# Performance work log

Measured on AMD Instinct MI355X. Metric: run time of the kernel, lower is better.

## Reference

```python
import math
import jax, jax.numpy as jnp
import numpy as np

GRID = (256, 256, 256)
K = 9                # kernel_size (already odd)
SIGMA = K / 4.0
PAD = K // 2
CLIP = 0.03


def _gaussian_kernel():
    ax = np.arange(K, dtype=np.float32)
    mean = (K - 1) / 2.0
    g = np.exp(-(((ax - mean) / SIGMA) ** 2) / 2.0) / (SIGMA * math.sqrt(2.0 * math.pi))
    k = g[:, None, None] * g[None, :, None] * g[None, None, :]
    k = k / k.sum()
    return jnp.asarray(k, dtype=jnp.float32).reshape(1, 1, K, K, K)  # OIDHW


def setup_inputs() -> dict:
    key = jax.random.key(0)
    x = jax.random.normal(key, (int(np.prod(GRID)),), dtype=jnp.float32)
    kernel = _gaussian_kernel()
    return {"x": x, "kernel": kernel}


def reference(x, kernel):
    v = x.reshape(1, 1, *GRID)  # [1,1,D,H,W]
    # reflect padding (torch padding_mode='reflect', padding = K//2)
    p = jnp.pad(v, ((0, 0), (0, 0), (PAD, PAD), (PAD, PAD), (PAD, PAD)), mode="reflect")
    # torch Conv3d is cross-correlation; lax conv does not flip kernels either
    out = jax.lax.conv_general_dilated(
        p, kernel,
        window_strides=(1, 1, 1),
        padding="VALID",
        dimension_numbers=("NCDHW", "OIDHW", "NCDHW"),
    )
    # clip: keep smoothed output within +/-CLIP of the original input
    out = jnp.maximum(jnp.minimum(v, out + CLIP), out - CLIP)
    return out.reshape(-1)
```

## Files before the change

kernel.cpp:

```cpp
#include <hip/hip_runtime.h>
#include <hip/hip_fp16.h>
#include <math.h>

#define CLIPV 0.03f

struct W9 { float g[9]; };
struct half4 { __half2 a, b; };

__device__ __forceinline__ int reflect_idx(int i, int n) {
    if (i < 0) i = -i;
    if (i >= n) i = 2 * n - 2 - i;
    return i;
}

__device__ __forceinline__ float4 h4_to_f4(half4 v) {
    const float2 ab = __half22float2(v.a), cd = __half22float2(v.b);
    float4 r; r.x = ab.x; r.y = ab.y; r.z = cd.x; r.w = cd.y; return r;
}
__device__ __forceinline__ half4 f4_to_h4(float4 v) {
    half4 r; r.a = __floats2half2_rn(v.x, v.y); r.b = __floats2half2_rn(v.z, v.w);
    return r;
}

__global__ __launch_bounds__(256) void wh_pass(const float* __restrict__ x,
                                               __half* __restrict__ t2, W9 wt) {
    __shared__ __half tile[64][264];

    const int bid = blockIdx.x;
    const int xcd = bid & 7;
    const int k   = bid >> 3;
    const int z   = xcd * 32 + (k >> 2);
    const int rb  = (k & 3) * 64;
    const int wv  = threadIdx.x >> 6;
    const int h0  = rb + wv * 16;
    const int L   = threadIdx.x & 63;
    const int w4  = L * 4;

    const float* plane = x + (size_t)z * 65536;

    {
        float4 ring[9];
        float4 cur = *(const float4*)(plane + (size_t)reflect_idx(h0 - 4, 256) * 256 + w4);
        float4 nxt = *(const float4*)(plane + (size_t)reflect_idx(h0 - 3, 256) * 256 + w4);

        #pragma unroll
        for (int i = 0; i < 24; ++i) {
            float4 nn;
            if (i < 22)
                nn = *(const float4*)(plane + (size_t)reflect_idx(h0 - 2 + i, 256) * 256 + w4);

            ring[i % 9] = cur;

            if (i >= 8) {
                float a0 = 0.f, a1 = 0.f, a2 = 0.f, a3 = 0.f;
                #pragma unroll
                for (int j = 0; j < 9; ++j) {
                    const float4 v = ring[(i - 8 + j) % 9];
                    a0 = fmaf(wt.g[j], v.x, a0);
                    a1 = fmaf(wt.g[j], v.y, a1);
                    a2 = fmaf(wt.g[j], v.z, a2);
                    a3 = fmaf(wt.g[j], v.w, a3);
                }
                float4 o; o.x = a0; o.y = a1; o.z = a2; o.w = a3;
                *(half4*)&tile[wv * 16 + (i - 8)][w4] = f4_to_h4(o);
            }

            cur = nxt; nxt = nn;
        }
    }
    __syncthreads();

    __half* oplane = t2 + (size_t)z * 65536 + (size_t)rb * 256;
    const bool l0 = (L == 0), l63 = (L == 63);
    const int offA = l0  ? w4 : (w4 - 4);
    const int offC = l63 ? w4 : (w4 + 4);

    #pragma unroll
    for (int s = 0; s < 16; ++s) {
        const int r = wv * 16 + s;
        const float4 A = h4_to_f4(*(const half4*)&tile[r][offA]);
        const float4 B = h4_to_f4(*(const half4*)&tile[r][w4]);
        const float4 C = h4_to_f4(*(const half4*)&tile[r][offC]);

        float sv[12];
        sv[0] = l0 ? C.x : A.x;
        sv[1] = l0 ? B.w : A.y;
        sv[2] = l0 ? B.z : A.z;
        sv[3] = l0 ? B.y : A.w;
        sv[4] = B.x; sv[5] = B.y; sv[6] = B.z; sv[7] = B.w;
        sv[8]  = l63 ? B.z : C.x;
        sv[9]  = l63 ? B.y : C.y;
        sv[10] = l63 ? B.x : C.z;
        sv[11] = l63 ? A.w : C.w;

        float a0 = 0.f, a1 = 0.f, a2 = 0.f, a3 = 0.f;
        #pragma unroll
        for (int j = 0; j < 9; ++j) {
            a0 = fmaf(wt.g[j], sv[j],     a0);
            a1 = fmaf(wt.g[j], sv[j + 1], a1);
            a2 = fmaf(wt.g[j], sv[j + 2], a2);
            a3 = fmaf(wt.g[j], sv[j + 3], a3);
        }
        float4 o; o.x = a0; o.y = a1; o.z = a2; o.w = a3;
        *(half4*)(oplane + (size_t)r * 256 + w4) = f4_to_h4(o);
    }
}

__global__ __launch_bounds__(256) void d_clip_pass(const __half* __restrict__ t2,
                                                   const float* __restrict__ x,
                                                   float* __restrict__ out, W9 wt) {
    const int bid   = blockIdx.x;
    const int xcd   = bid & 7;
    const int k     = bid >> 3;
    const int chunk = xcd * 2 + (k & 1);
    const int tile  = k >> 1;
    const int z0    = chunk * 16;
    const size_t c4 = (size_t)tile * 256 + threadIdx.x;

    const half4*  t4 = (const half4*)t2;
    const float4* xp = (const float4*)x;
    float4*       o4 = (float4*)out;

    float4 ring[9];

    half4 cur = t4[(size_t)reflect_idx(z0 - 4, 256) * 16384 + c4];
    half4 nxt = t4[(size_t)reflect_idx(z0 - 3, 256) * 16384 + c4];
    float4 xCur, xNxt;

    #pragma unroll
    for (int i = 0; i < 24; ++i) {
        half4 nn;
        if (i < 22)
            nn = t4[(size_t)reflect_idx(z0 - 2 + i, 256) * 16384 + c4];
        float4 xNew;
        if (i >= 6 && i < 22)
            xNew = xp[(size_t)(z0 + i - 6) * 16384 + c4];

        ring[i % 9] = h4_to_f4(cur);

        if (i >= 8) {
            const int z = z0 + i - 8;
            float a0 = 0.f, a1 = 0.f, a2 = 0.f, a3 = 0.f;
            #pragma unroll
            for (int j = 0; j < 9; ++j) {
                const float4 v = ring[(i - 8 + j) % 9];
                a0 = fmaf(wt.g[j], v.x, a0);
                a1 = fmaf(wt.g[j], v.y, a1);
                a2 = fmaf(wt.g[j], v.z, a2);
                a3 = fmaf(wt.g[j], v.w, a3);
            }
            const float4 xv = xCur;
            float4 r;
            r.x = fmaxf(fminf(xv.x, a0 + CLIPV), a0 - CLIPV);
            r.y = fmaxf(fminf(xv.y, a1 + CLIPV), a1 - CLIPV);
            r.z = fmaxf(fminf(xv.z, a2 + CLIPV), a2 - CLIPV);
            r.w = fmaxf(fminf(xv.w, a3 + CLIPV), a3 - CLIPV);
            o4[(size_t)z * 16384 + c4] = r;
        }

        cur = nxt; nxt = nn;
        xCur = xNxt; xNxt = xNew;
    }
}

extern "C" void kernel_launch(void* const* d_in, const int* in_sizes, int n_in,
                              void* d_out, int out_size, void* d_ws, size_t ws_size,
                              hipStream_t stream) {
    const float* x = (const float*)d_in[0];
    float* out = (float*)d_out;
    __half* t2 = (__half*)d_ws;

    W9 wt;
    {
        double g[9], s = 0.0;
        const double sigma = 9.0 / 4.0;
        for (int i = 0; i < 9; ++i) {
            double tt = (i - 4.0) / sigma;
            g[i] = exp(-0.5 * tt * tt);
            s += g[i];
        }
        for (int i = 0; i < 9; ++i) wt.g[i] = (float)(g[i] / s);
    }

    wh_pass<<<dim3(1024), dim3(256), 0, stream>>>(x, t2, wt);
    d_clip_pass<<<dim3(1024), dim3(256), 0, stream>>>(t2, x, out, wt);
}
```

Measured before the change: 53.67 us.

## Reorder WH pass to W-then-H with async global-to-LDS row streaming

```diff
diff --git a/kernel.cpp b/kernel.cpp
--- a/kernel.cpp
+++ b/kernel.cpp
@@ -24,63 +24,49 @@
 
 __global__ __launch_bounds__(256) void wh_pass(const float* __restrict__ x,
                                                __half* __restrict__ t2, W9 wt) {
-    __shared__ __half tile[64][264];
+    __shared__ float stage[4][4][256];
 
     const int bid = blockIdx.x;
     const int xcd = bid & 7;
     const int k   = bid >> 3;
     const int z   = xcd * 32 + (k >> 2);
-    const int rb  = (k & 3) * 64;
     const int wv  = threadIdx.x >> 6;
-    const int h0  = rb + wv * 16;
+    const int h0  = ((k & 3) * 4 + wv) * 16;
     const int L   = threadIdx.x & 63;
     const int w4  = L * 4;
+    const bool l0 = (L == 0), l63 = (L == 63);
 
-    const float* plane = x + (size_t)z * 65536;
+    const float* plane  = x  + (size_t)z * 65536;
+    __half*      oplane = t2 + (size_t)z * 65536;
 
-    {
-        float4 ring[9];
-        float4 cur = *(const float4*)(plane + (size_t)reflect_idx(h0 - 4, 256) * 256 + w4);
-        float4 nxt = *(const float4*)(plane + (size_t)reflect_idx(h0 - 3, 256) * 256 + w4);
+    auto dma_row = [&](int i, int slot) {
+        const float* src = plane + (size_t)reflect_idx(h0 - 4 + i, 256) * 256 + w4;
+        __builtin_amdgcn_global_load_lds(
+            (const __attribute__((address_space(1))) unsigned int*)src,
+            (__attribute__((address_space(3))) unsigned int*)&stage[wv][slot][0],
+            16, 0, 0);
+    };
 
-        #pragma unroll
-        for (int i = 0; i < 24; ++i) {
-            float4 nn;
-            if (i < 22)
-                nn = *(const float4*)(plane + (size_t)reflect_idx(h0 - 2 + i, 256) * 256 + w4);
+    float4 ring[9];
 
-            ring[i % 9] = cur;
+    dma_row(0, 0);
+    dma_row(1, 1);
 
-            if (i >= 8) {
-                float a0 = 0.f, a1 = 0.f, a2 = 0.f, a3 = 0.f;
-                #pragma unroll
-                for (int j = 0; j < 9; ++j) {
-                    const float4 v = ring[(i - 8 + j) % 9];
-                    a0 = fmaf(wt.g[j], v.x, a0);
-                    a1 = fmaf(wt.g[j], v.y, a1);
-                    a2 = fmaf(wt.g[j], v.z, a2);
-                    a3 = fmaf(wt.g[j], v.w, a3);
-                }
-                float4 o; o.x = a0; o.y = a1; o.z = a2; o.w = a3;
-                *(half4*)&tile[wv * 16 + (i - 8)][w4] = f4_to_h4(o);
-            }
-
-            cur = nxt; nxt = nn;
-        }
-    }
-    __syncthreads();
-
-    __half* oplane = t2 + (size_t)z * 65536 + (size_t)rb * 256;
-    const bool l0 = (L == 0), l63 = (L == 63);
     const int offA = l0  ? w4 : (w4 - 4);
     const int offC = l63 ? w4 : (w4 + 4);
 
     #pragma unroll
-    for (int s = 0; s < 16; ++s) {
-        const int r = wv * 16 + s;
-        const float4 A = h4_to_f4(*(const half4*)&tile[r][offA]);
-        const float4 B = h4_to_f4(*(const half4*)&tile[r][w4]);
-        const float4 C = h4_to_f4(*(const half4*)&tile[r][offC]);
+    for (int i = 0; i < 24; ++i) {
+        if (i < 22) dma_row(i + 2, (i + 2) & 3);
+
+        if (i <= 8 || i == 23) asm volatile("s_waitcnt vmcnt(2)" ::: "memory");
+        else                   asm volatile("s_waitcnt vmcnt(3)" ::: "memory");
+        __builtin_amdgcn_sched_barrier(0);
+
+        const float* rowp = &stage[wv][i & 3][0];
+        const float4 A = *(const float4*)(rowp + offA);
+        const float4 B = *(const float4*)(rowp + w4);
+        const float4 C = *(const float4*)(rowp + offC);
 
         float sv[12];
         sv[0] = l0 ? C.x : A.x;
@@ -93,16 +79,32 @@
         sv[10] = l63 ? B.x : C.z;
         sv[11] = l63 ? A.w : C.w;
 
-        float a0 = 0.f, a1 = 0.f, a2 = 0.f, a3 = 0.f;
-        #pragma unroll
-        for (int j = 0; j < 9; ++j) {
-            a0 = fmaf(wt.g[j], sv[j],     a0);
-            a1 = fmaf(wt.g[j], sv[j + 1], a1);
-            a2 = fmaf(wt.g[j], sv[j + 2], a2);
-            a3 = fmaf(wt.g[j], sv[j + 3], a3);
+        {
+            float a0 = 0.f, a1 = 0.f, a2 = 0.f, a3 = 0.f;
+            #pragma unroll
+            for (int j = 0; j < 9; ++j) {
+                a0 = fmaf(wt.g[j], sv[j],     a0);
+                a1 = fmaf(wt.g[j], sv[j + 1], a1);
+                a2 = fmaf(wt.g[j], sv[j + 2], a2);
+                a3 = fmaf(wt.g[j], sv[j + 3], a3);
+            }
+            float4 wc; wc.x = a0; wc.y = a1; wc.z = a2; wc.w = a3;
+            ring[i % 9] = wc;
         }
-        float4 o; o.x = a0; o.y = a1; o.z = a2; o.w = a3;
-        *(half4*)(oplane + (size_t)r * 256 + w4) = f4_to_h4(o);
+
+        if (i >= 8) {
+            float a0 = 0.f, a1 = 0.f, a2 = 0.f, a3 = 0.f;
+            #pragma unroll
+            for (int j = 0; j < 9; ++j) {
+                const float4 v = ring[(i - 8 + j) % 9];
+                a0 = fmaf(wt.g[j], v.x, a0);
+                a1 = fmaf(wt.g[j], v.y, a1);
+                a2 = fmaf(wt.g[j], v.z, a2);
+                a3 = fmaf(wt.g[j], v.w, a3);
+            }
+            float4 o; o.x = a0; o.y = a1; o.z = a2; o.w = a3;
+            *(half4*)(oplane + (size_t)(h0 + i - 8) * 256 + w4) = f4_to_h4(o);
+        }
     }
 }
 
```

After: 52.91 us. Within noise of the previous version (-1.4%).
